# Performance work log

Hardware: AMD Instinct MI355X
Metric: run time of the kernel (lower is better)

Reference implementation:

```python
import jax, jax.numpy as jnp
import numpy as np

N, E, V, D = 40000, 1280000, 5000, 256
H1, C1 = 8, 32   # conv1: 8 heads x 32 -> concat 256
H2, C2 = 4, 64   # conv2: 4 heads x 64 -> concat 256
B, NC = 64, 20
EPS = 1e-5


def setup_inputs():
    key = jax.random.key(0)
    ks = jax.random.split(key, 16)
    def nrm(k, shape, s=0.05):
        return jax.random.normal(k, shape, jnp.float32) * s
    return {
        "x": jax.random.normal(ks[0], (N, V), jnp.float32),
        "edge_index": jax.random.randint(ks[1], (2, E), 0, N, dtype=jnp.int32),
        "batch": jax.random.randint(ks[2], (N,), 0, B, dtype=jnp.int32),
        "W_in": nrm(ks[3], (V, D)), "b_in": jnp.zeros((D,), jnp.float32),
        "W1": nrm(ks[4], (D, H1 * C1)),
        "att_src1": nrm(ks[5], (H1, C1)), "att_dst1": nrm(ks[6], (H1, C1)),
        "b1": jnp.zeros((H1 * C1,), jnp.float32),
        "g1": jnp.ones((D,), jnp.float32), "be1": jnp.zeros((D,), jnp.float32),
        "W2": nrm(ks[7], (D, H2 * C2)),
        "att_src2": nrm(ks[8], (H2, C2)), "att_dst2": nrm(ks[9], (H2, C2)),
        "b2": jnp.zeros((H2 * C2,), jnp.float32),
        "g2": jnp.ones((D,), jnp.float32), "be2": jnp.zeros((D,), jnp.float32),
        "Wf": nrm(ks[10], (2 * D, D)), "bf": jnp.zeros((D,), jnp.float32),
        "Wc1": nrm(ks[11], (D, D // 2)), "bc1": jnp.zeros((D // 2,), jnp.float32),
        "Wc2": nrm(ks[12], (D // 2, NC)), "bc2": jnp.zeros((NC,), jnp.float32),
    }


def gat_conv(x, src, dst, W, a_src, a_dst, bias, H, C):
    n = x.shape[0]
    h = (x @ W).reshape(n, H, C)                     # [N,H,C]
    s_src = (h * a_src).sum(-1)                      # [N,H]
    s_dst = (h * a_dst).sum(-1)                      # [N,H]
    e = jax.nn.leaky_relu(s_src[src] + s_dst[dst], 0.2)  # [Etot,H]
    # per-destination softmax (self-loops guarantee nonempty segments)
    m = jax.ops.segment_max(e, dst, num_segments=n)
    p = jnp.exp(e - m[dst])
    z = jax.ops.segment_sum(p, dst, num_segments=n)
    alpha = p / z[dst]
    out = jax.ops.segment_sum(alpha[:, :, None] * h[src], dst, num_segments=n)
    return out.reshape(n, H * C) + bias


def layer_norm(x, g, b):
    mu = x.mean(-1, keepdims=True)
    var = ((x - mu) ** 2).mean(-1, keepdims=True)
    return (x - mu) * jax.lax.rsqrt(var + EPS) * g + b


def reference(x, edge_index, batch, W_in, b_in, W1, att_src1, att_dst1, b1, g1, be1,
              W2, att_src2, att_dst2, b2, g2, be2, Wf, bf, Wc1, bc1, Wc2, bc2):
    n = x.shape[0]
    loops = jnp.arange(n, dtype=edge_index.dtype)
    src = jnp.concatenate([edge_index[0], loops])    # add_self_loops=True
    dst = jnp.concatenate([edge_index[1], loops])

    x0 = x @ W_in + b_in                             # input_proj
    h = jax.nn.elu(gat_conv(x0, src, dst, W1, att_src1, att_dst1, b1, H1, C1))
    x1 = layer_norm(h + x0, g1, be1)
    h = jax.nn.elu(gat_conv(x1, src, dst, W2, att_src2, att_dst2, b2, H2, C2))
    x2 = layer_norm(h + x1, g2, be2)

    cnt = jax.ops.segment_sum(jnp.ones((n,), x.dtype), batch, num_segments=B)
    cnt = jnp.maximum(cnt, 1.0)[:, None]
    x_global = jax.ops.segment_sum(x2, batch, num_segments=B) / cnt
    x_skip = jax.ops.segment_sum(x0, batch, num_segments=B) / cnt

    xc = jnp.concatenate([x_global, x_skip], axis=-1)
    f = jax.nn.relu(xc @ Wf + bf)
    logits = jax.nn.relu(f @ Wc1 + bc1) @ Wc2 + bc2
    return jax.nn.log_softmax(logits, axis=1)
```

## Files before the change

kernel.cpp:

```cpp
#include <hip/hip_runtime.h>
#include <stdint.h>

#define N_NODES 40000
#define M_PAD   40064
#define V_DIM   5000
#define K1_PAD  5024
#define E_EDGES 1280000
#define B_BATCH 64
#define NCLS    20

typedef __attribute__((ext_vector_type(8))) short bf16x8;
typedef __attribute__((ext_vector_type(4))) float f32x4;

__device__ __forceinline__ unsigned short f2bf(float x) {
    union { float f; unsigned int u; } c; c.f = x;
    unsigned int u = c.u;
    unsigned int r = (u + 0x7FFFu + ((u >> 16) & 1u)) >> 16;
    return (unsigned short)r;
}

__global__ void prep_bt(const float* __restrict__ W, unsigned short* __restrict__ BT,
                        int K, int K_pad, int N)
{
    int idx = blockIdx.x * 256 + threadIdx.x;
    int total = N * K_pad;
    if (idx >= total) return;
    int n = idx / K_pad;
    int k = idx - n * K_pad;
    float v = (k < K) ? W[(size_t)k * N + n] : 0.f;
    BT[idx] = f2bf(v);
}

__global__ __launch_bounds__(256)
void gemm_bf16(const float* __restrict__ A, const unsigned short* __restrict__ BT,
               float* __restrict__ C, const float* __restrict__ bias,
               int M_real, int K_real, int K_pad)
{
    __shared__ unsigned short As[128 * 32];
    __shared__ unsigned short Bs[128 * 32];
    const int m0 = blockIdx.x * 128;
    const int n0 = blockIdx.y * 128;
    const int t = threadIdx.x;
    const int lane = t & 63;
    const int wave = t >> 6;
    const int wr = (wave >> 1) * 64;
    const int wc = (wave & 1) * 64;
    const int lm = lane & 15;
    const int lk = (lane >> 4) * 8;

    f32x4 acc[4][4];
#pragma unroll
    for (int i = 0; i < 4; i++)
#pragma unroll
        for (int j = 0; j < 4; j++) {
            acc[i][j][0] = 0.f; acc[i][j][1] = 0.f;
            acc[i][j][2] = 0.f; acc[i][j][3] = 0.f;
        }

    const int nkt = K_pad >> 5;
    for (int kt = 0; kt < nkt; ++kt) {
        const int k0 = kt << 5;
#pragma unroll
        for (int i = 0; i < 4; i++) {
            int lin = t + (i << 8);
            int r = lin >> 3;
            int cs = lin & 7;
            int row = m0 + r;
            int k = k0 + (cs << 2);
            float v0 = 0.f, v1 = 0.f, v2 = 0.f, v3 = 0.f;
            if (row < M_real) {
                if (k + 4 <= K_real) {
                    const float4 v = *(const float4*)(A + (size_t)row * K_real + k);
                    v0 = v.x; v1 = v.y; v2 = v.z; v3 = v.w;
                } else {
                    const float* ap = A + (size_t)row * K_real;
                    if (k + 0 < K_real) v0 = ap[k + 0];
                    if (k + 1 < K_real) v1 = ap[k + 1];
                    if (k + 2 < K_real) v2 = ap[k + 2];
                    if (k + 3 < K_real) v3 = ap[k + 3];
                }
            }
            uint2 pk;
            pk.x = (unsigned int)f2bf(v0) | ((unsigned int)f2bf(v1) << 16);
            pk.y = (unsigned int)f2bf(v2) | ((unsigned int)f2bf(v3) << 16);
            *(uint2*)&As[r * 32 + (cs << 2)] = pk;
        }
#pragma unroll
        for (int i = 0; i < 2; i++) {
            int lin = t + (i << 8);
            int r = lin >> 2;
            int seg = lin & 3;
            const uint4 v = *(const uint4*)(BT + (size_t)(n0 + r) * K_pad + k0 + (seg << 3));
            *(uint4*)&Bs[r * 32 + (seg << 3)] = v;
        }
        __syncthreads();

        bf16x8 af[4], bfr[4];
#pragma unroll
        for (int i = 0; i < 4; i++)
            af[i] = *(const bf16x8*)&As[(wr + i * 16 + lm) * 32 + lk];
#pragma unroll
        for (int j = 0; j < 4; j++)
            bfr[j] = *(const bf16x8*)&Bs[(wc + j * 16 + lm) * 32 + lk];
#pragma unroll
        for (int i = 0; i < 4; i++)
#pragma unroll
            for (int j = 0; j < 4; j++)
                acc[i][j] = __builtin_amdgcn_mfma_f32_16x16x32_bf16(af[i], bfr[j], acc[i][j], 0, 0, 0);
        __syncthreads();
    }

    const int lrow = (lane >> 4) * 4;
#pragma unroll
    for (int i = 0; i < 4; i++) {
        int rowb = m0 + wr + i * 16 + lrow;
#pragma unroll
        for (int j = 0; j < 4; j++) {
            int col = n0 + wc + j * 16 + lm;
            float badd = bias ? bias[col] : 0.f;
#pragma unroll
            for (int r = 0; r < 4; r++)
                C[(size_t)(rowb + r) * 256 + col] = acc[i][j][r] + badd;
        }
    }
}

__global__ void deg_init(int* __restrict__ deg, int n) {
    int i = blockIdx.x * 256 + threadIdx.x;
    if (i < n) deg[i] = 1;
}
__global__ void count_kernel(const int* __restrict__ ei, int* __restrict__ deg, int E) {
    int e = blockIdx.x * 256 + threadIdx.x;
    if (e < E) atomicAdd(&deg[ei[E + e]], 1);
}
__global__ void scan_kernel(const int* __restrict__ deg, int* __restrict__ row_start, int n) {
    __shared__ int sm[1024];
    __shared__ int carry;
    int t = threadIdx.x;
    if (t == 0) carry = 0;
    __syncthreads();
    for (int base = 0; base < n; base += 1024) {
        int v = (base + t < n) ? deg[base + t] : 0;
        sm[t] = v;
        __syncthreads();
        for (int off = 1; off < 1024; off <<= 1) {
            int y = (t >= off) ? sm[t - off] : 0;
            __syncthreads();
            sm[t] += y;
            __syncthreads();
        }
        int c = carry;
        if (base + t < n) row_start[base + t] = c + sm[t] - v;
        __syncthreads();
        if (t == 1023) carry = c + sm[1023];
        __syncthreads();
    }
    if (t == 0) row_start[n] = carry;
}
__global__ void selfloop_kernel(const int* __restrict__ row_start, int* __restrict__ cursor,
                                int* __restrict__ nbr, int n) {
    int i = blockIdx.x * 256 + threadIdx.x;
    if (i < n) { int rs = row_start[i]; nbr[rs] = i; cursor[i] = rs + 1; }
}
__global__ void scatter_kernel(const int* __restrict__ ei, int* __restrict__ cursor,
                               int* __restrict__ nbr, int E) {
    int e = blockIdx.x * 256 + threadIdx.x;
    if (e < E) {
        int s = ei[e], d = ei[E + e];
        int pos = atomicAdd(&cursor[d], 1);
        nbr[pos] = s;
    }
}

__global__ void batch_count(const int* __restrict__ batch, float* __restrict__ cnt, int n) {
    int i = blockIdx.x * 256 + threadIdx.x;
    if (i < n) atomicAdd(&cnt[batch[i]], 1.f);
}
__global__ void pool_kernel(const float* __restrict__ x, const int* __restrict__ batch,
                            float* __restrict__ sums) {
    int node = blockIdx.x;
    int t = threadIdx.x;
    int b = batch[node];
    atomicAdd(&sums[b * 256 + t], x[(size_t)node * 256 + t]);
}

template <int H, int C>
__global__ __launch_bounds__(256)
void attn_scores(const float* __restrict__ hbuf, const float* __restrict__ a_src,
                 const float* __restrict__ a_dst, float* __restrict__ s_src,
                 float* __restrict__ s_dst)
{
    const int node = blockIdx.x;
    const int t = threadIdx.x;
    float hv = hbuf[(size_t)node * 256 + t];
    float ps = hv * a_src[t];
    float pd = hv * a_dst[t];
#pragma unroll
    for (int off = C / 2; off >= 1; off >>= 1) {
        ps += __shfl_down(ps, off, 64);
        pd += __shfl_down(pd, off, 64);
    }
    if ((t & (C - 1)) == 0) {
        s_src[node * H + t / C] = ps;
        s_dst[node * H + t / C] = pd;
    }
}

template <int H, int C>
__global__ __launch_bounds__(256)
void gat_kernel(const float* __restrict__ hbuf, const float* __restrict__ s_src,
                const float* __restrict__ s_dst, const int* __restrict__ row_start,
                const int* __restrict__ nbr, const float* __restrict__ bias,
                const float* __restrict__ gamma, const float* __restrict__ beta,
                const float* __restrict__ x_in, float* __restrict__ x_out)
{
    const int node = blockIdx.x;
    const int t = threadIdx.x;
    const int head = t / C;
    const float sd = s_dst[node * H + head];
    const int beg = row_start[node], end = row_start[node + 1];

    float m = -3.4e38f, z = 0.f, acc = 0.f;
    for (int p = beg; p < end; ++p) {
        int s = nbr[p];
        float e = s_src[s * H + head] + sd;
        e = (e > 0.f) ? e : 0.2f * e;
        float hv = hbuf[(size_t)s * 256 + t];
        float mn = fmaxf(m, e);
        float scale = __expf(m - mn);
        float pe = __expf(e - mn);
        z = z * scale + pe;
        acc = acc * scale + pe * hv;
        m = mn;
    }
    float v = acc / z + bias[t];
    v = (v > 0.f) ? v : (__expf(v) - 1.f);
    v += x_in[(size_t)node * 256 + t];

    __shared__ float sbuf[256];
    sbuf[t] = v; __syncthreads();
    for (int s2 = 128; s2 > 0; s2 >>= 1) { if (t < s2) sbuf[t] += sbuf[t + s2]; __syncthreads(); }
    float mu = sbuf[0] * (1.f / 256.f);
    __syncthreads();
    float d = v - mu;
    sbuf[t] = d * d; __syncthreads();
    for (int s2 = 128; s2 > 0; s2 >>= 1) { if (t < s2) sbuf[t] += sbuf[t + s2]; __syncthreads(); }
    float var = sbuf[0] * (1.f / 256.f);
    x_out[(size_t)node * 256 + t] = d * rsqrtf(var + 1e-5f) * gamma[t] + beta[t];
}

__global__ __launch_bounds__(256)
void mlp_head(const float* __restrict__ xg_sum, const float* __restrict__ xs_sum,
              const float* __restrict__ cnt,
              const float* __restrict__ Wf, const float* __restrict__ bfv,
              const float* __restrict__ Wc1, const float* __restrict__ bc1,
              const float* __restrict__ Wc2, const float* __restrict__ bc2,
              float* __restrict__ out)
{
    const int b = blockIdx.x;
    const int t = threadIdx.x;
    __shared__ float xc[512];
    __shared__ float fs[256];
    __shared__ float gs[128];
    __shared__ float logits[NCLS];
    float c = fmaxf(cnt[b], 1.f);
    xc[t]       = xg_sum[b * 256 + t] / c;
    xc[256 + t] = xs_sum[b * 256 + t] / c;
    __syncthreads();
    float a = bfv[t];
    for (int i = 0; i < 512; i++) a += xc[i] * Wf[i * 256 + t];
    fs[t] = fmaxf(a, 0.f);
    __syncthreads();
    if (t < 128) {
        float a1 = bc1[t];
        for (int i = 0; i < 256; i++) a1 += fs[i] * Wc1[i * 128 + t];
        gs[t] = fmaxf(a1, 0.f);
    }
    __syncthreads();
    if (t < NCLS) {
        float a2 = bc2[t];
        for (int i = 0; i < 128; i++) a2 += gs[i] * Wc2[i * NCLS + t];
        logits[t] = a2;
    }
    __syncthreads();
    if (t < NCLS) {
        float mx = -3.4e38f;
        for (int i = 0; i < NCLS; i++) mx = fmaxf(mx, logits[i]);
        float s = 0.f;
        for (int i = 0; i < NCLS; i++) s += expf(logits[i] - mx);
        out[b * NCLS + t] = logits[t] - mx - logf(s);
    }
}

extern "C" void kernel_launch(void* const* d_in, const int* in_sizes, int n_in,
                              void* d_out, int out_size, void* d_ws, size_t ws_size,
                              hipStream_t stream)
{
    const float* x      = (const float*)d_in[0];
    const int*   ei     = (const int*)d_in[1];
    const int*   batch  = (const int*)d_in[2];
    const float* W_in   = (const float*)d_in[3];
    const float* b_in   = (const float*)d_in[4];
    const float* W1     = (const float*)d_in[5];
    const float* att_s1 = (const float*)d_in[6];
    const float* att_d1 = (const float*)d_in[7];
    const float* b1     = (const float*)d_in[8];
    const float* g1     = (const float*)d_in[9];
    const float* be1    = (const float*)d_in[10];
    const float* W2     = (const float*)d_in[11];
    const float* att_s2 = (const float*)d_in[12];
    const float* att_d2 = (const float*)d_in[13];
    const float* b2     = (const float*)d_in[14];
    const float* g2     = (const float*)d_in[15];
    const float* be2    = (const float*)d_in[16];
    const float* Wf     = (const float*)d_in[17];
    const float* bfv    = (const float*)d_in[18];
    const float* Wc1    = (const float*)d_in[19];
    const float* bc1    = (const float*)d_in[20];
    const float* Wc2    = (const float*)d_in[21];
    const float* bc2    = (const float*)d_in[22];
    float* out = (float*)d_out;

    char* ws = (char*)d_ws;
    size_t off = 0;
    auto alloc = [&](size_t bytes) -> char* {
        char* p = ws + off;
        off += (bytes + 255) & ~(size_t)255;
        return p;
    };
    float* x0 = (float*)alloc((size_t)M_PAD * 256 * 4);
    float* hb = (float*)alloc((size_t)M_PAD * 256 * 4);
    float* x1 = (float*)alloc((size_t)M_PAD * 256 * 4);
    unsigned short* BTin = (unsigned short*)alloc((size_t)256 * K1_PAD * 2);
    unsigned short* BT1  = (unsigned short*)alloc((size_t)256 * 256 * 2);
    unsigned short* BT2  = (unsigned short*)alloc((size_t)256 * 256 * 2);
    float* s_src = (float*)alloc((size_t)N_NODES * 8 * 4);
    float* s_dst = (float*)alloc((size_t)N_NODES * 8 * 4);
    int* deg       = (int*)alloc((size_t)N_NODES * 4);
    int* row_start = (int*)alloc((size_t)(N_NODES + 1) * 4);
    int* cursor    = (int*)alloc((size_t)N_NODES * 4);
    int* nbr       = (int*)alloc((size_t)(E_EDGES + N_NODES) * 4);
    float* xs_sum  = (float*)alloc(64 * 256 * 4);
    float* xg_sum  = (float*)alloc(64 * 256 * 4);
    float* cnt     = (float*)alloc(64 * 4);
    float* x2 = x0;

    hipMemsetAsync(xs_sum, 0, 64 * 256 * 4, stream);
    hipMemsetAsync(xg_sum, 0, 64 * 256 * 4, stream);
    hipMemsetAsync(cnt, 0, 64 * 4, stream);

    prep_bt<<<(256 * K1_PAD + 255) / 256, 256, 0, stream>>>(W_in, BTin, V_DIM, K1_PAD, 256);
    prep_bt<<<(256 * 256 + 255) / 256, 256, 0, stream>>>(W1, BT1, 256, 256, 256);
    prep_bt<<<(256 * 256 + 255) / 256, 256, 0, stream>>>(W2, BT2, 256, 256, 256);
    deg_init<<<(N_NODES + 255) / 256, 256, 0, stream>>>(deg, N_NODES);
    count_kernel<<<(E_EDGES + 255) / 256, 256, 0, stream>>>(ei, deg, E_EDGES);
    scan_kernel<<<1, 1024, 0, stream>>>(deg, row_start, N_NODES);
    selfloop_kernel<<<(N_NODES + 255) / 256, 256, 0, stream>>>(row_start, cursor, nbr, N_NODES);
    scatter_kernel<<<(E_EDGES + 255) / 256, 256, 0, stream>>>(ei, cursor, nbr, E_EDGES);
    batch_count<<<(N_NODES + 255) / 256, 256, 0, stream>>>(batch, cnt, N_NODES);

    gemm_bf16<<<dim3(313, 2), 256, 0, stream>>>(x, BTin, x0, b_in, N_NODES, V_DIM, K1_PAD);
    pool_kernel<<<N_NODES, 256, 0, stream>>>(x0, batch, xs_sum);

    gemm_bf16<<<dim3(313, 2), 256, 0, stream>>>(x0, BT1, hb, nullptr, N_NODES, 256, 256);
    attn_scores<8, 32><<<N_NODES, 256, 0, stream>>>(hb, att_s1, att_d1, s_src, s_dst);
    gat_kernel<8, 32><<<N_NODES, 256, 0, stream>>>(hb, s_src, s_dst, row_start, nbr,
                                                   b1, g1, be1, x0, x1);
    gemm_bf16<<<dim3(313, 2), 256, 0, stream>>>(x1, BT2, hb, nullptr, N_NODES, 256, 256);
    attn_scores<4, 64><<<N_NODES, 256, 0, stream>>>(hb, att_s2, att_d2, s_src, s_dst);
    gat_kernel<4, 64><<<N_NODES, 256, 0, stream>>>(hb, s_src, s_dst, row_start, nbr,
                                                   b2, g2, be2, x1, x2);

    pool_kernel<<<N_NODES, 256, 0, stream>>>(x2, batch, xg_sum);
    mlp_head<<<B_BATCH, 256, 0, stream>>>(xg_sum, xs_sum, cnt, Wf, bfv, Wc1, bc1, Wc2, bc2, out);
}
```

Baseline: 2.518 ms.

## Rework GEMM pipeline, store projections in bf16, replace atomic pooling with partial reductions

Several changes land together. The GEMM now uses a K=64 tile with an XOR-swizzled LDS layout and register prefetch of the next tile. Its output for the GAT projections is written as bf16, which halves the gather traffic in the attention and aggregation kernels. The weight-transpose kernel is replaced by an LDS-tiled version, the CSR scan uses wave shuffles, the GAT loop prefetches the next neighbor, and per-node atomic pooling becomes block-partial sums plus a reduction. Storing the projections in bf16 lowers the precision of the gathered features.

```diff
diff --git a/kernel.cpp b/kernel.cpp
--- a/kernel.cpp
+++ b/kernel.cpp
@@ -1,13 +1,16 @@
 #include <hip/hip_runtime.h>
+#include <hip/hip_bf16.h>
 #include <stdint.h>
 
 #define N_NODES 40000
 #define M_PAD   40064
 #define V_DIM   5000
-#define K1_PAD  5024
+#define K1_PAD  5056
 #define E_EDGES 1280000
 #define B_BATCH 64
 #define NCLS    20
+#define POOL_BLOCKS 160
+#define POOL_NPER   250
 
 typedef __attribute__((ext_vector_type(8))) short bf16x8;
 typedef __attribute__((ext_vector_type(4))) float f32x4;
@@ -18,26 +21,49 @@
     unsigned int r = (u + 0x7FFFu + ((u >> 16) & 1u)) >> 16;
     return (unsigned short)r;
 }
-
-__global__ void prep_bt(const float* __restrict__ W, unsigned short* __restrict__ BT,
-                        int K, int K_pad, int N)
-{
-    int idx = blockIdx.x * 256 + threadIdx.x;
-    int total = N * K_pad;
-    if (idx >= total) return;
-    int n = idx / K_pad;
-    int k = idx - n * K_pad;
-    float v = (k < K) ? W[(size_t)k * N + n] : 0.f;
-    BT[idx] = f2bf(v);
+__device__ __forceinline__ float bf2f(unsigned short b) {
+    union { unsigned int u; float f; } c; c.u = ((unsigned int)b) << 16; return c.f;
+}
+__device__ __forceinline__ unsigned int pk_bf16(float a, float b) {
+    __hip_bfloat162 h = __float22bfloat162_rn(make_float2(a, b));
+    union { __hip_bfloat162 v; unsigned int u; } cv; cv.v = h; return cv.u;
+}
+
+__global__ __launch_bounds__(256)
+void transpose_cvt(const float* __restrict__ W, unsigned short* __restrict__ BT,
+                   int K, int N, int K_pad)
+{
+    __shared__ float tile[64][65];
+    const int t = threadIdx.x;
+    const int k0 = blockIdx.x * 64, n0 = blockIdx.y * 64;
+    const int tn = t & 63, tk = t >> 6;
+#pragma unroll
+    for (int r = 0; r < 64; r += 4) {
+        int k = k0 + tk + r;
+        tile[tk + r][tn] = (k < K) ? W[(size_t)k * N + n0 + tn] : 0.f;
+    }
+    __syncthreads();
+    const int blk = t & 7;
+#pragma unroll
+    for (int i = 0; i < 2; ++i) {
+        int row = (t >> 3) + i * 32;
+        uint4 pa;
+        pa.x = pk_bf16(tile[blk * 8 + 0][row], tile[blk * 8 + 1][row]);
+        pa.y = pk_bf16(tile[blk * 8 + 2][row], tile[blk * 8 + 3][row]);
+        pa.z = pk_bf16(tile[blk * 8 + 4][row], tile[blk * 8 + 5][row]);
+        pa.w = pk_bf16(tile[blk * 8 + 6][row], tile[blk * 8 + 7][row]);
+        *(uint4*)(BT + (size_t)(n0 + row) * K_pad + k0 + blk * 8) = pa;
+    }
 }
 
 __global__ __launch_bounds__(256)
 void gemm_bf16(const float* __restrict__ A, const unsigned short* __restrict__ BT,
-               float* __restrict__ C, const float* __restrict__ bias,
-               int M_real, int K_real, int K_pad)
-{
-    __shared__ unsigned short As[128 * 32];
-    __shared__ unsigned short Bs[128 * 32];
+               float* __restrict__ Cf, unsigned short* __restrict__ Cb,
+               const float* __restrict__ bias,
+               int M_clamp, int K_real, int K_pad)
+{
+    __shared__ unsigned short As[128 * 64];
+    __shared__ unsigned short Bs[128 * 64];
     const int m0 = blockIdx.x * 128;
     const int n0 = blockIdx.y * 128;
     const int t = threadIdx.x;
@@ -46,81 +72,101 @@
     const int wr = (wave >> 1) * 64;
     const int wc = (wave & 1) * 64;
     const int lm = lane & 15;
-    const int lk = (lane >> 4) * 8;
+    const int lkq = lane >> 4;
+    const int blk = t & 7;
+    const int r0 = t >> 3;
+
+    float4 ra[8];
+    uint4 rb[4];
+
+    auto loadA = [&](int k0) {
+        int k = k0 + blk * 8;
+        bool valid = (k < K_real);
+#pragma unroll
+        for (int i = 0; i < 4; ++i) {
+            int gr = m0 + r0 + i * 32;
+            gr = gr < M_clamp ? gr : M_clamp;
+            const float* p = A + (size_t)gr * K_real + k;
+            if (valid) { ra[2 * i] = *(const float4*)p; ra[2 * i + 1] = *(const float4*)(p + 4); }
+            else       { ra[2 * i] = make_float4(0, 0, 0, 0); ra[2 * i + 1] = make_float4(0, 0, 0, 0); }
+        }
+    };
+    auto loadB = [&](int k0) {
+        int k = k0 + blk * 8;
+#pragma unroll
+        for (int i = 0; i < 4; ++i)
+            rb[i] = *(const uint4*)(BT + (size_t)(n0 + r0 + i * 32) * K_pad + k);
+    };
+    auto stage = [&]() {
+#pragma unroll
+        for (int i = 0; i < 4; ++i) {
+            int row = r0 + i * 32;
+            int phys = blk ^ (row & 7);
+            uint4 pa;
+            pa.x = pk_bf16(ra[2 * i].x, ra[2 * i].y);
+            pa.y = pk_bf16(ra[2 * i].z, ra[2 * i].w);
+            pa.z = pk_bf16(ra[2 * i + 1].x, ra[2 * i + 1].y);
+            pa.w = pk_bf16(ra[2 * i + 1].z, ra[2 * i + 1].w);
+            *(uint4*)&As[row * 64 + phys * 8] = pa;
+            *(uint4*)&Bs[row * 64 + phys * 8] = rb[i];
+        }
+    };
 
     f32x4 acc[4][4];
 #pragma unroll
     for (int i = 0; i < 4; i++)
 #pragma unroll
         for (int j = 0; j < 4; j++) {
-            acc[i][j][0] = 0.f; acc[i][j][1] = 0.f;
-            acc[i][j][2] = 0.f; acc[i][j][3] = 0.f;
-        }
-
-    const int nkt = K_pad >> 5;
+            acc[i][j][0] = 0.f; acc[i][j][1] = 0.f; acc[i][j][2] = 0.f; acc[i][j][3] = 0.f;
+        }
+
+    loadA(0); loadB(0);
+    const int nkt = K_pad >> 6;
     for (int kt = 0; kt < nkt; ++kt) {
-        const int k0 = kt << 5;
-#pragma unroll
-        for (int i = 0; i < 4; i++) {
-            int lin = t + (i << 8);
-            int r = lin >> 3;
-            int cs = lin & 7;
-            int row = m0 + r;
-            int k = k0 + (cs << 2);
-            float v0 = 0.f, v1 = 0.f, v2 = 0.f, v3 = 0.f;
-            if (row < M_real) {
-                if (k + 4 <= K_real) {
-                    const float4 v = *(const float4*)(A + (size_t)row * K_real + k);
-                    v0 = v.x; v1 = v.y; v2 = v.z; v3 = v.w;
-                } else {
-                    const float* ap = A + (size_t)row * K_real;
-                    if (k + 0 < K_real) v0 = ap[k + 0];
-                    if (k + 1 < K_real) v1 = ap[k + 1];
-                    if (k + 2 < K_real) v2 = ap[k + 2];
-                    if (k + 3 < K_real) v3 = ap[k + 3];
-                }
+        stage();
+        __syncthreads();
+        if (kt + 1 < nkt) { loadA((kt + 1) << 6); loadB((kt + 1) << 6); }
+#pragma unroll
+        for (int kh = 0; kh < 2; ++kh) {
+            bf16x8 af[4], bfr[4];
+#pragma unroll
+            for (int i = 0; i < 4; ++i) {
+                int row = wr + i * 16 + lm;
+                int phys = (kh * 4 + lkq) ^ (row & 7);
+                af[i] = *(const bf16x8*)&As[row * 64 + phys * 8];
             }
-            uint2 pk;
-            pk.x = (unsigned int)f2bf(v0) | ((unsigned int)f2bf(v1) << 16);
-            pk.y = (unsigned int)f2bf(v2) | ((unsigned int)f2bf(v3) << 16);
-            *(uint2*)&As[r * 32 + (cs << 2)] = pk;
-        }
-#pragma unroll
-        for (int i = 0; i < 2; i++) {
-            int lin = t + (i << 8);
-            int r = lin >> 2;
-            int seg = lin & 3;
-            const uint4 v = *(const uint4*)(BT + (size_t)(n0 + r) * K_pad + k0 + (seg << 3));
-            *(uint4*)&Bs[r * 32 + (seg << 3)] = v;
-        }
-        __syncthreads();
-
-        bf16x8 af[4], bfr[4];
-#pragma unroll
-        for (int i = 0; i < 4; i++)
-            af[i] = *(const bf16x8*)&As[(wr + i * 16 + lm) * 32 + lk];
-#pragma unroll
-        for (int j = 0; j < 4; j++)
-            bfr[j] = *(const bf16x8*)&Bs[(wc + j * 16 + lm) * 32 + lk];
-#pragma unroll
-        for (int i = 0; i < 4; i++)
-#pragma unroll
-            for (int j = 0; j < 4; j++)
-                acc[i][j] = __builtin_amdgcn_mfma_f32_16x16x32_bf16(af[i], bfr[j], acc[i][j], 0, 0, 0);
+#pragma unroll
+            for (int j = 0; j < 4; ++j) {
+                int row = wc + j * 16 + lm;
+                int phys = (kh * 4 + lkq) ^ (row & 7);
+                bfr[j] = *(const bf16x8*)&Bs[row * 64 + phys * 8];
+            }
+#pragma unroll
+            for (int i = 0; i < 4; ++i)
+#pragma unroll
+                for (int j = 0; j < 4; ++j)
+                    acc[i][j] = __builtin_amdgcn_mfma_f32_16x16x32_bf16(af[i], bfr[j], acc[i][j], 0, 0, 0);
+        }
         __syncthreads();
     }
 
     const int lrow = (lane >> 4) * 4;
 #pragma unroll
-    for (int i = 0; i < 4; i++) {
+    for (int i = 0; i < 4; ++i) {
         int rowb = m0 + wr + i * 16 + lrow;
 #pragma unroll
-        for (int j = 0; j < 4; j++) {
+        for (int j = 0; j < 4; ++j) {
             int col = n0 + wc + j * 16 + lm;
-            float badd = bias ? bias[col] : 0.f;
-#pragma unroll
-            for (int r = 0; r < 4; r++)
-                C[(size_t)(rowb + r) * 256 + col] = acc[i][j][r] + badd;
+            if (Cf) {
+                float badd = bias ? bias[col] : 0.f;
+#pragma unroll
+                for (int r = 0; r < 4; ++r)
+                    Cf[(size_t)(rowb + r) * 256 + col] = acc[i][j][r] + badd;
+            } else {
+#pragma unroll
+                for (int r = 0; r < 4; ++r)
+                    Cb[(size_t)(rowb + r) * 256 + col] = f2bf(acc[i][j][r]);
+            }
         }
     }
 }
@@ -134,28 +180,40 @@
     if (e < E) atomicAdd(&deg[ei[E + e]], 1);
 }
 __global__ void scan_kernel(const int* __restrict__ deg, int* __restrict__ row_start, int n) {
-    __shared__ int sm[1024];
-    __shared__ int carry;
-    int t = threadIdx.x;
-    if (t == 0) carry = 0;
+    __shared__ int sws[16];
+    __shared__ int carry_s;
+    const int t = threadIdx.x, lane = t & 63, w = t >> 6;
+    if (t == 0) carry_s = 0;
     __syncthreads();
     for (int base = 0; base < n; base += 1024) {
-        int v = (base + t < n) ? deg[base + t] : 0;
-        sm[t] = v;
-        __syncthreads();
-        for (int off = 1; off < 1024; off <<= 1) {
-            int y = (t >= off) ? sm[t - off] : 0;
-            __syncthreads();
-            sm[t] += y;
-            __syncthreads();
-        }
-        int c = carry;
-        if (base + t < n) row_start[base + t] = c + sm[t] - v;
-        __syncthreads();
-        if (t == 1023) carry = c + sm[1023];
-        __syncthreads();
-    }
-    if (t == 0) row_start[n] = carry;
+        int i = base + t;
+        int v = (i < n) ? deg[i] : 0;
+        int incl = v;
+#pragma unroll
+        for (int off = 1; off < 64; off <<= 1) {
+            int y = __shfl_up(incl, off, 64);
+            if (lane >= off) incl += y;
+        }
+        if (lane == 63) sws[w] = incl;
+        __syncthreads();
+        if (t < 16) {
+            int x = sws[t];
+#pragma unroll
+            for (int off = 1; off < 16; off <<= 1) {
+                int y = __shfl_up(x, off, 16);
+                if ((t & 15) >= off) x += y;
+            }
+            sws[t] = x;
+        }
+        __syncthreads();
+        int c = carry_s;
+        int waveoff = (w > 0) ? sws[w - 1] : 0;
+        if (i < n) row_start[i] = c + waveoff + incl - v;
+        __syncthreads();
+        if (t == 0) carry_s = c + sws[15];
+        __syncthreads();
+    }
+    if (t == 0) row_start[n] = carry_s;
 }
 __global__ void selfloop_kernel(const int* __restrict__ row_start, int* __restrict__ cursor,
                                 int* __restrict__ nbr, int n) {
@@ -176,23 +234,40 @@
     int i = blockIdx.x * 256 + threadIdx.x;
     if (i < n) atomicAdd(&cnt[batch[i]], 1.f);
 }
-__global__ void pool_kernel(const float* __restrict__ x, const int* __restrict__ batch,
-                            float* __restrict__ sums) {
-    int node = blockIdx.x;
-    int t = threadIdx.x;
-    int b = batch[node];
-    atomicAdd(&sums[b * 256 + t], x[(size_t)node * 256 + t]);
+__global__ __launch_bounds__(256)
+void pool_partial(const float* __restrict__ x, const int* __restrict__ batch,
+                  float* __restrict__ partial)
+{
+    __shared__ float acc[64 * 256];
+    const int t = threadIdx.x;
+#pragma unroll
+    for (int i = 0; i < 64; ++i) acc[i * 256 + t] = 0.f;
+    int nbeg = blockIdx.x * POOL_NPER;
+    int nend = nbeg + POOL_NPER; if (nend > N_NODES) nend = N_NODES;
+    for (int node = nbeg; node < nend; ++node) {
+        int b = batch[node];
+        acc[b * 256 + t] += x[(size_t)node * 256 + t];
+    }
+    float* dst = partial + (size_t)blockIdx.x * 64 * 256;
+#pragma unroll 4
+    for (int i = 0; i < 64; ++i) dst[i * 256 + t] = acc[i * 256 + t];
+}
+__global__ void pool_reduce(const float* __restrict__ partial, float* __restrict__ sums) {
+    int b = blockIdx.x, t = threadIdx.x;
+    float s = 0.f;
+    for (int k = 0; k < POOL_BLOCKS; ++k) s += partial[(size_t)k * 16384 + b * 256 + t];
+    sums[b * 256 + t] = s;
 }
 
 template <int H, int C>
 __global__ __launch_bounds__(256)
-void attn_scores(const float* __restrict__ hbuf, const float* __restrict__ a_src,
+void attn_scores(const unsigned short* __restrict__ hb, const float* __restrict__ a_src,
                  const float* __restrict__ a_dst, float* __restrict__ s_src,
                  float* __restrict__ s_dst)
 {
     const int node = blockIdx.x;
     const int t = threadIdx.x;
-    float hv = hbuf[(size_t)node * 256 + t];
+    float hv = bf2f(hb[(size_t)node * 256 + t]);
     float ps = hv * a_src[t];
     float pd = hv * a_dst[t];
 #pragma unroll
@@ -208,7 +283,7 @@
 
 template <int H, int C>
 __global__ __launch_bounds__(256)
-void gat_kernel(const float* __restrict__ hbuf, const float* __restrict__ s_src,
+void gat_kernel(const unsigned short* __restrict__ hb, const float* __restrict__ s_src,
                 const float* __restrict__ s_dst, const int* __restrict__ row_start,
                 const int* __restrict__ nbr, const float* __restrict__ bias,
                 const float* __restrict__ gamma, const float* __restrict__ beta,
@@ -221,16 +296,23 @@
     const int beg = row_start[node], end = row_start[node + 1];
 
     float m = -3.4e38f, z = 0.f, acc = 0.f;
+    int s0 = nbr[beg];
+    float sr_n = s_src[s0 * H + head];
+    float hv_n = bf2f(hb[(size_t)s0 * 256 + t]);
     for (int p = beg; p < end; ++p) {
-        int s = nbr[p];
-        float e = s_src[s * H + head] + sd;
+        float sr = sr_n, hv = hv_n;
+        if (p + 1 < end) {
+            int s1 = nbr[p + 1];
+            sr_n = s_src[s1 * H + head];
+            hv_n = bf2f(hb[(size_t)s1 * 256 + t]);
+        }
+        float e = sr + sd;
         e = (e > 0.f) ? e : 0.2f * e;
-        float hv = hbuf[(size_t)s * 256 + t];
         float mn = fmaxf(m, e);
-        float scale = __expf(m - mn);
+        float sc = __expf(m - mn);
         float pe = __expf(e - mn);
-        z = z * scale + pe;
-        acc = acc * scale + pe * hv;
+        z = z * sc + pe;
+        acc = acc * sc + pe * hv;
         m = mn;
     }
     float v = acc / z + bias[t];
@@ -329,8 +411,8 @@
         return p;
     };
     float* x0 = (float*)alloc((size_t)M_PAD * 256 * 4);
-    float* hb = (float*)alloc((size_t)M_PAD * 256 * 4);
     float* x1 = (float*)alloc((size_t)M_PAD * 256 * 4);
+    unsigned short* hb = (unsigned short*)alloc((size_t)M_PAD * 256 * 2);
     unsigned short* BTin = (unsigned short*)alloc((size_t)256 * K1_PAD * 2);
     unsigned short* BT1  = (unsigned short*)alloc((size_t)256 * 256 * 2);
     unsigned short* BT2  = (unsigned short*)alloc((size_t)256 * 256 * 2);
@@ -340,18 +422,17 @@
     int* row_start = (int*)alloc((size_t)(N_NODES + 1) * 4);
     int* cursor    = (int*)alloc((size_t)N_NODES * 4);
     int* nbr       = (int*)alloc((size_t)(E_EDGES + N_NODES) * 4);
+    float* partial = (float*)alloc((size_t)POOL_BLOCKS * 64 * 256 * 4);
     float* xs_sum  = (float*)alloc(64 * 256 * 4);
     float* xg_sum  = (float*)alloc(64 * 256 * 4);
     float* cnt     = (float*)alloc(64 * 4);
     float* x2 = x0;
 
-    hipMemsetAsync(xs_sum, 0, 64 * 256 * 4, stream);
-    hipMemsetAsync(xg_sum, 0, 64 * 256 * 4, stream);
     hipMemsetAsync(cnt, 0, 64 * 4, stream);
 
-    prep_bt<<<(256 * K1_PAD + 255) / 256, 256, 0, stream>>>(W_in, BTin, V_DIM, K1_PAD, 256);
-    prep_bt<<<(256 * 256 + 255) / 256, 256, 0, stream>>>(W1, BT1, 256, 256, 256);
-    prep_bt<<<(256 * 256 + 255) / 256, 256, 0, stream>>>(W2, BT2, 256, 256, 256);
+    transpose_cvt<<<dim3(K1_PAD / 64, 4), 256, 0, stream>>>(W_in, BTin, V_DIM, 256, K1_PAD);
+    transpose_cvt<<<dim3(4, 4), 256, 0, stream>>>(W1, BT1, 256, 256, 256);
+    transpose_cvt<<<dim3(4, 4), 256, 0, stream>>>(W2, BT2, 256, 256, 256);
     deg_init<<<(N_NODES + 255) / 256, 256, 0, stream>>>(deg, N_NODES);
     count_kernel<<<(E_EDGES + 255) / 256, 256, 0, stream>>>(ei, deg, E_EDGES);
     scan_kernel<<<1, 1024, 0, stream>>>(deg, row_start, N_NODES);
@@ -359,18 +440,20 @@
     scatter_kernel<<<(E_EDGES + 255) / 256, 256, 0, stream>>>(ei, cursor, nbr, E_EDGES);
     batch_count<<<(N_NODES + 255) / 256, 256, 0, stream>>>(batch, cnt, N_NODES);
 
-    gemm_bf16<<<dim3(313, 2), 256, 0, stream>>>(x, BTin, x0, b_in, N_NODES, V_DIM, K1_PAD);
-    pool_kernel<<<N_NODES, 256, 0, stream>>>(x0, batch, xs_sum);
-
-    gemm_bf16<<<dim3(313, 2), 256, 0, stream>>>(x0, BT1, hb, nullptr, N_NODES, 256, 256);
+    gemm_bf16<<<dim3(313, 2), 256, 0, stream>>>(x, BTin, x0, nullptr, b_in, N_NODES - 1, V_DIM, K1_PAD);
+    pool_partial<<<POOL_BLOCKS, 256, 0, stream>>>(x0, batch, partial);
+    pool_reduce<<<B_BATCH, 256, 0, stream>>>(partial, xs_sum);
+
+    gemm_bf16<<<dim3(313, 2), 256, 0, stream>>>(x0, BT1, nullptr, hb, nullptr, M_PAD - 1, 256, 256);
     attn_scores<8, 32><<<N_NODES, 256, 0, stream>>>(hb, att_s1, att_d1, s_src, s_dst);
     gat_kernel<8, 32><<<N_NODES, 256, 0, stream>>>(hb, s_src, s_dst, row_start, nbr,
                                                    b1, g1, be1, x0, x1);
-    gemm_bf16<<<dim3(313, 2), 256, 0, stream>>>(x1, BT2, hb, nullptr, N_NODES, 256, 256);
+    gemm_bf16<<<dim3(313, 2), 256, 0, stream>>>(x1, BT2, nullptr, hb, nullptr, M_PAD - 1, 256, 256);
     attn_scores<4, 64><<<N_NODES, 256, 0, stream>>>(hb, att_s2, att_d2, s_src, s_dst);
     gat_kernel<4, 64><<<N_NODES, 256, 0, stream>>>(hb, s_src, s_dst, row_start, nbr,
                                                    b2, g2, be2, x1, x2);
 
-    pool_kernel<<<N_NODES, 256, 0, stream>>>(x2, batch, xg_sum);
+    pool_partial<<<POOL_BLOCKS, 256, 0, stream>>>(x2, batch, partial);
+    pool_reduce<<<B_BATCH, 256, 0, stream>>>(partial, xg_sum);
     mlp_head<<<B_BATCH, 256, 0, stream>>>(xg_sum, xs_sum, cnt, Wf, bfv, Wc1, bc1, Wc2, bc2, out);
 }
```

Measured after the change: 2.735 ms. 1.09x slower.
